# Kernel tuning notes

Measured on AMD Instinct MI355X. Metric: run time of the kernel, lower is better.

## Reference

```python
import jax, jax.numpy as jnp
import numpy as np

EMB = 128  # embsize
WORD = 128  # word_size
ITERS = 2


def _agg(embeds, neibors):
    # embeds: [B, N, D], neibors: [B, N, K] indices into node axis N (per batch)
    # mean-pool gathered neighbor embeddings -> [B, N, D]
    gathered = jax.vmap(lambda e, idx: e[idx])(embeds, neibors)  # [B, N, K, D]
    return gathered.mean(axis=2)


def setup_inputs() -> dict:
    key = jax.random.key(0)
    ks = jax.random.split(key, 9)
    B, N, K = 64, 512, 16
    word_embs = jax.random.normal(ks[0], (B, N, WORD), dtype=jnp.float32)
    lib_embs = jax.random.normal(ks[1], (B, N, WORD), dtype=jnp.float32)
    neibors = jax.random.randint(ks[2], (B, N, K), 0, N)
    neibors_lib = jax.random.randint(ks[3], (B, N, K), 0, N)
    mask = jax.random.uniform(ks[4], (B, N), dtype=jnp.float32)
    # xavier-uniform style params
    def xav(k, shape):
        bound = float(np.sqrt(6.0 / (shape[0] + shape[1])))
        return jax.random.uniform(k, shape, dtype=jnp.float32, minval=-bound, maxval=bound)
    weight = xav(ks[5], (WORD, EMB))
    weight2 = xav(ks[6], (EMB, EMB))
    enc_w1 = xav(ks[7], (WORD, EMB))
    enc_w2 = xav(ks[8], (EMB, EMB))
    return {"word_embs": word_embs, "neibors": neibors, "lib_embs": lib_embs,
            "neibors_lib": neibors_lib, "mask": mask, "weight": weight,
            "weight2": weight2, "enc_w1": enc_w1, "enc_w2": enc_w2}


def reference(word_embs, neibors, lib_embs, neibors_lib, mask, weight, weight2, enc_w1, enc_w2):
    B, N, _ = word_embs.shape
    # lib aggregation is loop-invariant (lib_embs fixed); same math as in-loop recompute
    agg_lib = jnp.einsum('bnw,we->bne', _agg(lib_embs, neibors_lib), weight)  # [B, N, EMB]
    word_proj = jnp.einsum('bnw,we->bne', word_embs, enc_w1)  # loop-invariant
    last_embed = jnp.zeros((B, N, EMB), dtype=jnp.float32)
    for _ in range(ITERS):
        agg_func = _agg(last_embed, neibors)  # [B, N, EMB]
        last_embed = jnp.tanh(word_proj + jnp.einsum('bne,ef->bnf', agg_func, enc_w2) + agg_lib)
    # masked sum over nodes, then final linear
    pooled = (last_embed * mask[:, :, None]).sum(axis=1)  # [B, EMB]
    return pooled @ weight2
```

## Files before the change

kernel.cpp:

```cpp
#include <hip/hip_runtime.h>
#include <hip/hip_bf16.h>

#define B_    64
#define N_    512
#define K_    16
#define D_    128
#define NPBLK 128
#define GG    ((B_*N_)/NPBLK)

typedef float f32x4  __attribute__((ext_vector_type(4)));
typedef short bf16x8 __attribute__((ext_vector_type(8)));

static __device__ __forceinline__ short f2bf(float x) {
    union { float f; unsigned u; } v; v.f = x;
    unsigned r = v.u + 0x7fffu + ((v.u >> 16) & 1u);
    return (short)(r >> 16);
}
static __device__ __forceinline__ float bf2f(short h) {
    return __uint_as_float(((unsigned)(unsigned short)h) << 16);
}
static __device__ __forceinline__ float fast_tanh(float x) {
    float e = __expf(2.f * x);
    return 1.f - 2.f * __builtin_amdgcn_rcpf(e + 1.f);
}

__global__ __launch_bounds__(256) void pack(const float* __restrict__ enc1,
                                            const float* __restrict__ wgt,
                                            const float* __restrict__ enc2,
                                            short* __restrict__ Bp1e,
                                            short* __restrict__ Bpw,
                                            short* __restrict__ Bp2,
                                            float* __restrict__ out) {
    const int blk = blockIdx.x, t = threadIdx.x;
    if (blk >= 24) { out[(blk - 24) * 256 + t] = 0.f; return; }
    const int ptid = blk * 256 + t;
    const int m3 = ptid >> 11;
    const int r = ptid & 2047;
    const int ks = r >> 9, nt = (r >> 6) & 7, l = r & 63;
    const int k0 = ks * 32 + (l >> 4) * 8;
    const int col = nt * 16 + (l & 15);
    const float* src = (m3 == 0) ? enc1 : (m3 == 1) ? wgt : enc2;
    const float scale = (m3 == 0) ? 1.0f : 0.0625f;
    short* dst = (m3 == 0) ? Bp1e : (m3 == 1) ? Bpw : Bp2;
    short o8[8];
#pragma unroll
    for (int j = 0; j < 8; ++j) o8[j] = f2bf(src[(k0 + j) * 128 + col] * scale);
    *(int4*)&dst[(size_t)r * 8] = *(int4*)o8;
}

static __device__ __forceinline__ int swz_blk() {
    const int hw = blockIdx.x;
    return ((hw & 7) << 5) + (hw >> 3);
}

static __device__ __forceinline__ int lds_addr(int row, int colb) {
    return (row * 256 + colb) ^ ((row & 7) << 4);
}

__global__ __launch_bounds__(512, 2) void g1(const float* __restrict__ word,
                                             const int* __restrict__ nbrL,
                                             const float* __restrict__ lib,
                                             const short* __restrict__ Bp1e,
                                             const short* __restrict__ Bpw,
                                             short* __restrict__ baseh,
                                             short* __restrict__ t1g) {
    extern __shared__ char smem[];
    short* sM  = (short*)smem;
    int*  sIdx = (int*)(smem + 131072);
    const int tid = threadIdx.x;
    const int logical = swz_blk();
    const int b = logical >> 2;
    const int node0 = (logical & 3) * NPBLK;
    const int gnode0 = b * N_ + node0;

    const float* libB = lib + (size_t)b * N_ * D_;
#pragma unroll 4
    for (int it = 0; it < 32; ++it) {
        const int i = it * 2048 + tid * 4;
        float4 v = *(const float4*)&libB[i];
        short4 s; s.x = f2bf(v.x); s.y = f2bf(v.y); s.z = f2bf(v.z); s.w = f2bf(v.w);
        *(short4*)(smem + lds_addr(i >> 7, (i & 127) * 2)) = s;
    }
    *(int4*)&sIdx[tid * 4] = *(const int4*)&nbrL[(size_t)gnode0 * 16 + tid * 4];
    __syncthreads();

    const int w = tid >> 6, l = tid & 63;
    const int nrow = w * 16 + (l & 15);
    int nidx[16];
#pragma unroll
    for (int nb = 0; nb < 16; ++nb) nidx[nb] = sIdx[nrow * 16 + nb];

    f32x4 acc[8];
#pragma unroll
    for (int nt = 0; nt < 8; ++nt) acc[nt] = (f32x4)0.f;

    bf16x8 bf[32];
#pragma unroll
    for (int q = 0; q < 32; ++q) bf[q] = *(const bf16x8*)&Bp1e[(size_t)(q * 64 + l) * 8];

    {
        const float* wr = word + (size_t)(gnode0 + nrow) * D_ + (l >> 4) * 8;
#pragma unroll
        for (int ks = 0; ks < 4; ++ks) {
            float4 a0 = *(const float4*)&wr[ks * 32];
            float4 a1 = *(const float4*)&wr[ks * 32 + 4];
            short af[8];
            af[0]=f2bf(a0.x); af[1]=f2bf(a0.y); af[2]=f2bf(a0.z); af[3]=f2bf(a0.w);
            af[4]=f2bf(a1.x); af[5]=f2bf(a1.y); af[6]=f2bf(a1.z); af[7]=f2bf(a1.w);
            bf16x8 av = *(bf16x8*)af;
#pragma unroll
            for (int nt = 0; nt < 8; ++nt)
                acc[nt] = __builtin_amdgcn_mfma_f32_16x16x32_bf16(av, bf[ks * 8 + nt], acc[nt], 0, 0, 0);
        }
    }

#pragma unroll
    for (int q = 0; q < 32; ++q) bf[q] = *(const bf16x8*)&Bpw[(size_t)(q * 64 + l) * 8];

    const int laneoff = (l >> 4) * 16;
#pragma unroll
    for (int nb = 0; nb < 16; ++nb) {
        const int rbase = nidx[nb] * 256 + laneoff;
        const int swz = (nidx[nb] & 7) << 4;
#pragma unroll
        for (int ksq = 0; ksq < 4; ++ksq) {
            bf16x8 av = *(const bf16x8*)(smem + ((rbase + ksq * 64) ^ swz));
#pragma unroll
            for (int nt = 0; nt < 8; ++nt)
                acc[nt] = __builtin_amdgcn_mfma_f32_16x16x32_bf16(av, bf[ksq * 8 + nt], acc[nt], 0, 0, 0);
        }
    }

    const int r0 = w * 16 + (l >> 4) * 4;
    const int cl = l & 15;
#pragma unroll
    for (int nt = 0; nt < 8; ++nt) {
        const int col = nt * 16 + cl;
#pragma unroll
        for (int r = 0; r < 4; ++r) {
            size_t o = (size_t)(gnode0 + r0 + r) * D_ + col;
            float v = acc[nt][r];
            baseh[o] = f2bf(v);
            t1g[o]   = f2bf(fast_tanh(v));
        }
    }
}

__global__ __launch_bounds__(512, 2) void g2(const short* __restrict__ t1g,
                                             const int* __restrict__ nbr,
                                             const short* __restrict__ Bp2,
                                             const short* __restrict__ baseh,
                                             const float* __restrict__ mask,
                                             const float* __restrict__ w2,
                                             float* __restrict__ out) {
    extern __shared__ char smem[];
    short* sM   = (short*)smem;
    int*  sIdx  = (int*)(smem + 131072);
    float* pred = (float*)(smem + 131072 + 8192);
    float* ptot = (float*)(smem + 131072 + 8192 + 4096);
    float* smask= (float*)(smem + 131072 + 8192 + 4096 + 512);
    const int tid = threadIdx.x;
    const int logical = swz_blk();
    const int b = logical >> 2;
    const int node0 = (logical & 3) * NPBLK;
    const int gnode0 = b * N_ + node0;

    const short* tB = t1g + (size_t)b * N_ * D_;
#pragma unroll 4
    for (int it = 0; it < 16; ++it) {
        const int i = it * 4096 + tid * 8;
        int4 v = *(const int4*)&tB[i];
        *(int4*)(smem + lds_addr(i >> 7, (i & 127) * 2)) = v;
    }
    *(int4*)&sIdx[tid * 4] = *(const int4*)&nbr[(size_t)gnode0 * 16 + tid * 4];
    if (tid < 128) smask[tid] = mask[gnode0 + tid];
    __syncthreads();

    const int w = tid >> 6, l = tid & 63;
    const int nrow = w * 16 + (l & 15);
    int nidx[16];
#pragma unroll
    for (int nb = 0; nb < 16; ++nb) nidx[nb] = sIdx[nrow * 16 + nb];

    f32x4 acc[8];
#pragma unroll
    for (int nt = 0; nt < 8; ++nt) acc[nt] = (f32x4)0.f;

    bf16x8 bf[32];
#pragma unroll
    for (int q = 0; q < 32; ++q) bf[q] = *(const bf16x8*)&Bp2[(size_t)(q * 64 + l) * 8];

    const int laneoff = (l >> 4) * 16;
#pragma unroll
    for (int nb = 0; nb < 16; ++nb) {
        const int rbase = nidx[nb] * 256 + laneoff;
        const int swz = (nidx[nb] & 7) << 4;
#pragma unroll
        for (int ksq = 0; ksq < 4; ++ksq) {
            bf16x8 av = *(const bf16x8*)(smem + ((rbase + ksq * 64) ^ swz));
#pragma unroll
            for (int nt = 0; nt < 8; ++nt)
                acc[nt] = __builtin_amdgcn_mfma_f32_16x16x32_bf16(av, bf[ksq * 8 + nt], acc[nt], 0, 0, 0);
        }
    }

    const int r0 = w * 16 + (l >> 4) * 4;
    const int cl = l & 15;
#pragma unroll
    for (int nt = 0; nt < 8; ++nt) {
        const int col = nt * 16 + cl;
        float s = 0.f;
#pragma unroll
        for (int r = 0; r < 4; ++r) {
            size_t o = (size_t)(gnode0 + r0 + r) * D_ + col;
            float v = fast_tanh(bf2f(baseh[o]) + acc[nt][r]);
            s += v * smask[r0 + r];
        }
        s += __shfl_xor(s, 16);
        s += __shfl_xor(s, 32);
        if (l < 16) pred[w * 128 + col] = s;
    }
    __syncthreads();
    if (tid < 128) {
        float tot = 0.f;
#pragma unroll
        for (int i = 0; i < 8; ++i) tot += pred[i * 128 + tid];
        ptot[tid] = tot;
    }
    __syncthreads();
    if (tid < 128) {
        float a2 = 0.f;
#pragma unroll 4
        for (int f = 0; f < 128; ++f) a2 += ptot[f] * w2[f * 128 + tid];
        atomicAdd(&out[b * 128 + tid], a2);
    }
}

extern "C" void kernel_launch(void* const* d_in, const int* in_sizes, int n_in,
                              void* d_out, int out_size, void* d_ws, size_t ws_size,
                              hipStream_t stream) {
    const float* word_embs   = (const float*)d_in[0];
    const int*   neibors     = (const int*)d_in[1];
    const float* lib_embs    = (const float*)d_in[2];
    const int*   neibors_lib = (const int*)d_in[3];
    const float* mask        = (const float*)d_in[4];
    const float* weight      = (const float*)d_in[5];
    const float* weight2     = (const float*)d_in[6];
    const float* enc_w1      = (const float*)d_in[7];
    const float* enc_w2      = (const float*)d_in[8];
    float* out = (float*)d_out;

    char* ws = (char*)d_ws;
    short* baseh = (short*)(ws);
    short* t1g   = (short*)(ws + (1u << 23));
    short* Bp1e  = (short*)(ws + (2u << 23));
    short* Bpw   = (short*)(ws + (2u << 23) + 32768);
    short* Bp2   = (short*)(ws + (2u << 23) + 65536);

    static int attr_done = 0;
    hipFuncSetAttribute((const void*)g1, hipFuncAttributeMaxDynamicSharedMemorySize, 139264);
    hipFuncSetAttribute((const void*)g2, hipFuncAttributeMaxDynamicSharedMemorySize, 144896);
    (void)attr_done;

    pack<<<56, 256, 0, stream>>>(enc_w1, weight, enc_w2, Bp1e, Bpw, Bp2, out);
    g1<<<GG, 512, 139264, stream>>>(word_embs, neibors_lib, lib_embs, Bp1e, Bpw, baseh, t1g);
    g2<<<GG, 512, 144896, stream>>>(t1g, neibors, Bp2, baseh, mask, weight2, out);
}
```

Before: 57.35 us.

## Aggregate neighbors before matmul and premultiply enc_w2 to shrink MFMA work

Uses linearity of the mean to sum gathered neighbor rows with packed fp32 adds first, then multiplies once. Previously every neighbor row was fed through the MFMA. In g1 the word projection and the lib aggregate share one K=256 GEMM. g1 also computes tanh(base)@enc_w2 and stores it, so g2 only gathers, sums, adds base, applies tanh and masks, with no matmul. This cuts MFMA work about 16x, in exchange for scalar gather-add work, an extra bf16 rounding of the intermediate, and B fragments loaded from global inside the loop instead of held in registers.

After: 55.75 us. -2.8%, faster.

```diff
diff --git a/kernel.cpp b/kernel.cpp
--- a/kernel.cpp
+++ b/kernel.cpp
@@ -3,10 +3,7 @@
 
 #define B_    64
 #define N_    512
-#define K_    16
 #define D_    128
-#define NPBLK 128
-#define GG    ((B_*N_)/NPBLK)
 
 typedef float f32x4  __attribute__((ext_vector_type(4)));
 typedef short bf16x8 __attribute__((ext_vector_type(8)));
@@ -16,12 +13,19 @@
     unsigned r = v.u + 0x7fffu + ((v.u >> 16) & 1u);
     return (short)(r >> 16);
 }
+static __device__ __forceinline__ float bfbits2f(unsigned hi_bits) {
+    return __uint_as_float(hi_bits);
+}
 static __device__ __forceinline__ float bf2f(short h) {
     return __uint_as_float(((unsigned)(unsigned short)h) << 16);
 }
 static __device__ __forceinline__ float fast_tanh(float x) {
     float e = __expf(2.f * x);
     return 1.f - 2.f * __builtin_amdgcn_rcpf(e + 1.f);
+}
+static __device__ __forceinline__ void pk_add(float2& acc, float x, float y) {
+    float2 v; v.x = x; v.y = y;
+    asm("v_pk_add_f32 %0, %1, %0" : "+v"(acc) : "v"(v));
 }
 
 __global__ __launch_bounds__(256) void pack(const float* __restrict__ enc1,
@@ -53,84 +57,110 @@
     return ((hw & 7) << 5) + (hw >> 3);
 }
 
-static __device__ __forceinline__ int lds_addr(int row, int colb) {
+static __device__ __forceinline__ int s_addr(int row, int colb) {
     return (row * 256 + colb) ^ ((row & 7) << 4);
 }
+
+#define LDA1 264
+#define LDA2 136
+#define T1OFF 69632
 
 __global__ __launch_bounds__(512, 2) void g1(const float* __restrict__ word,
                                              const int* __restrict__ nbrL,
                                              const float* __restrict__ lib,
                                              const short* __restrict__ Bp1e,
                                              const short* __restrict__ Bpw,
+                                             const short* __restrict__ Bp2,
                                              short* __restrict__ baseh,
-                                             short* __restrict__ t1g) {
+                                             short* __restrict__ u) {
     extern __shared__ char smem[];
-    short* sM  = (short*)smem;
-    int*  sIdx = (int*)(smem + 131072);
     const int tid = threadIdx.x;
     const int logical = swz_blk();
     const int b = logical >> 2;
-    const int node0 = (logical & 3) * NPBLK;
+    const int node0 = (logical & 3) * 128;
     const int gnode0 = b * N_ + node0;
 
     const float* libB = lib + (size_t)b * N_ * D_;
 #pragma unroll 4
-    for (int it = 0; it < 32; ++it) {
-        const int i = it * 2048 + tid * 4;
-        float4 v = *(const float4*)&libB[i];
-        short4 s; s.x = f2bf(v.x); s.y = f2bf(v.y); s.z = f2bf(v.z); s.w = f2bf(v.w);
-        *(short4*)(smem + lds_addr(i >> 7, (i & 127) * 2)) = s;
-    }
-    *(int4*)&sIdx[tid * 4] = *(const int4*)&nbrL[(size_t)gnode0 * 16 + tid * 4];
+    for (int it = 0; it < 16; ++it) {
+        const int i = it * 4096 + tid * 8;
+        float4 v0 = *(const float4*)&libB[i];
+        float4 v1 = *(const float4*)&libB[i + 4];
+        short o8[8];
+        o8[0]=f2bf(v0.x); o8[1]=f2bf(v0.y); o8[2]=f2bf(v0.z); o8[3]=f2bf(v0.w);
+        o8[4]=f2bf(v1.x); o8[5]=f2bf(v1.y); o8[6]=f2bf(v1.z); o8[7]=f2bf(v1.w);
+        *(int4*)(smem + s_addr(i >> 7, (i & 127) * 2)) = *(int4*)o8;
+    }
+    __syncthreads();
+
+    const int row = tid >> 2, cc = tid & 3;
+    int idxv[16];
+#pragma unroll
+    for (int q = 0; q < 4; ++q)
+        *(int4*)&idxv[q * 4] = *(const int4*)&nbrL[(size_t)(gnode0 + row) * 16 + q * 4];
+    float2 ac[16];
+#pragma unroll
+    for (int q = 0; q < 16; ++q) { ac[q].x = 0.f; ac[q].y = 0.f; }
+#pragma unroll
+    for (int nb = 0; nb < 16; ++nb) {
+        const int rr = idxv[nb];
+        const int sbase = rr * 256 + cc * 64;
+        const int sw = (rr & 7) << 4;
+#pragma unroll
+        for (int j = 0; j < 4; ++j) {
+            int4 d = *(const int4*)(smem + ((sbase + j * 16) ^ sw));
+            const unsigned* du = (const unsigned*)&d;
+#pragma unroll
+            for (int q = 0; q < 4; ++q) {
+                pk_add(ac[j * 4 + q], bfbits2f(du[q] << 16), bfbits2f(du[q] & 0xffff0000u));
+            }
+        }
+    }
+    __syncthreads();
+
+    short* sA = (short*)smem;
+    {
+        const float* wr = word + (size_t)(gnode0 + row) * D_ + cc * 32;
+#pragma unroll
+        for (int q = 0; q < 4; ++q) {
+            float4 v0 = *(const float4*)&wr[q * 8];
+            float4 v1 = *(const float4*)&wr[q * 8 + 4];
+            short o8[8];
+            o8[0]=f2bf(v0.x); o8[1]=f2bf(v0.y); o8[2]=f2bf(v0.z); o8[3]=f2bf(v0.w);
+            o8[4]=f2bf(v1.x); o8[5]=f2bf(v1.y); o8[6]=f2bf(v1.z); o8[7]=f2bf(v1.w);
+            *(int4*)&sA[row * LDA1 + cc * 32 + q * 8] = *(int4*)o8;
+        }
+#pragma unroll
+        for (int q = 0; q < 4; ++q) {
+            short o8[8];
+#pragma unroll
+            for (int m = 0; m < 4; ++m) {
+                o8[2*m]   = f2bf(ac[q * 4 + m].x);
+                o8[2*m+1] = f2bf(ac[q * 4 + m].y);
+            }
+            *(int4*)&sA[row * LDA1 + 128 + cc * 32 + q * 8] = *(int4*)o8;
+        }
+    }
     __syncthreads();
 
     const int w = tid >> 6, l = tid & 63;
-    const int nrow = w * 16 + (l & 15);
-    int nidx[16];
-#pragma unroll
-    for (int nb = 0; nb < 16; ++nb) nidx[nb] = sIdx[nrow * 16 + nb];
-
     f32x4 acc[8];
 #pragma unroll
     for (int nt = 0; nt < 8; ++nt) acc[nt] = (f32x4)0.f;
-
-    bf16x8 bf[32];
-#pragma unroll
-    for (int q = 0; q < 32; ++q) bf[q] = *(const bf16x8*)&Bp1e[(size_t)(q * 64 + l) * 8];
-
-    {
-        const float* wr = word + (size_t)(gnode0 + nrow) * D_ + (l >> 4) * 8;
-#pragma unroll
-        for (int ks = 0; ks < 4; ++ks) {
-            float4 a0 = *(const float4*)&wr[ks * 32];
-            float4 a1 = *(const float4*)&wr[ks * 32 + 4];
-            short af[8];
-            af[0]=f2bf(a0.x); af[1]=f2bf(a0.y); af[2]=f2bf(a0.z); af[3]=f2bf(a0.w);
-            af[4]=f2bf(a1.x); af[5]=f2bf(a1.y); af[6]=f2bf(a1.z); af[7]=f2bf(a1.w);
-            bf16x8 av = *(bf16x8*)af;
-#pragma unroll
-            for (int nt = 0; nt < 8; ++nt)
-                acc[nt] = __builtin_amdgcn_mfma_f32_16x16x32_bf16(av, bf[ks * 8 + nt], acc[nt], 0, 0, 0);
-        }
-    }
-
-#pragma unroll
-    for (int q = 0; q < 32; ++q) bf[q] = *(const bf16x8*)&Bpw[(size_t)(q * 64 + l) * 8];
-
-    const int laneoff = (l >> 4) * 16;
-#pragma unroll
-    for (int nb = 0; nb < 16; ++nb) {
-        const int rbase = nidx[nb] * 256 + laneoff;
-        const int swz = (nidx[nb] & 7) << 4;
-#pragma unroll
-        for (int ksq = 0; ksq < 4; ++ksq) {
-            bf16x8 av = *(const bf16x8*)(smem + ((rbase + ksq * 64) ^ swz));
-#pragma unroll
-            for (int nt = 0; nt < 8; ++nt)
-                acc[nt] = __builtin_amdgcn_mfma_f32_16x16x32_bf16(av, bf[ksq * 8 + nt], acc[nt], 0, 0, 0);
-        }
-    }
-
+    const int arow = w * 16 + (l & 15);
+#pragma unroll
+    for (int ks = 0; ks < 8; ++ks) {
+        bf16x8 a = *(const bf16x8*)&sA[arow * LDA1 + ks * 32 + (l >> 4) * 8];
+        const short* bp = (ks < 4) ? &Bp1e[((size_t)(ks * 8) * 64 + l) * 8]
+                                   : &Bpw[((size_t)((ks - 4) * 8) * 64 + l) * 8];
+#pragma unroll
+        for (int nt = 0; nt < 8; ++nt) {
+            bf16x8 bb = *(const bf16x8*)(bp + (size_t)nt * 64 * 8);
+            acc[nt] = __builtin_amdgcn_mfma_f32_16x16x32_bf16(a, bb, acc[nt], 0, 0, 0);
+        }
+    }
+
+    short* t1l = (short*)(smem + T1OFF);
     const int r0 = w * 16 + (l >> 4) * 4;
     const int cl = l & 15;
 #pragma unroll
@@ -138,93 +168,123 @@
         const int col = nt * 16 + cl;
 #pragma unroll
         for (int r = 0; r < 4; ++r) {
-            size_t o = (size_t)(gnode0 + r0 + r) * D_ + col;
+            const int grow = r0 + r;
             float v = acc[nt][r];
-            baseh[o] = f2bf(v);
-            t1g[o]   = f2bf(fast_tanh(v));
-        }
-    }
-}
-
-__global__ __launch_bounds__(512, 2) void g2(const short* __restrict__ t1g,
-                                             const int* __restrict__ nbr,
-                                             const short* __restrict__ Bp2,
+            baseh[(size_t)(gnode0 + grow) * D_ + col] = f2bf(v);
+            t1l[grow * LDA2 + col] = f2bf(fast_tanh(v));
+        }
+    }
+    __syncthreads();
+
+    f32x4 a2[8];
+#pragma unroll
+    for (int nt = 0; nt < 8; ++nt) a2[nt] = (f32x4)0.f;
+#pragma unroll
+    for (int ks = 0; ks < 4; ++ks) {
+        bf16x8 a = *(const bf16x8*)&t1l[arow * LDA2 + ks * 32 + (l >> 4) * 8];
+#pragma unroll
+        for (int nt = 0; nt < 8; ++nt) {
+            bf16x8 bb = *(const bf16x8*)&Bp2[((size_t)(ks * 8 + nt) * 64 + l) * 8];
+            a2[nt] = __builtin_amdgcn_mfma_f32_16x16x32_bf16(a, bb, a2[nt], 0, 0, 0);
+        }
+    }
+#pragma unroll
+    for (int nt = 0; nt < 8; ++nt) {
+        const int col = nt * 16 + cl;
+#pragma unroll
+        for (int r = 0; r < 4; ++r)
+            u[(size_t)(gnode0 + r0 + r) * D_ + col] = f2bf(a2[nt][r]);
+    }
+}
+
+__global__ __launch_bounds__(512, 2) void g2(const int* __restrict__ nbr,
+                                             const short* __restrict__ u,
                                              const short* __restrict__ baseh,
                                              const float* __restrict__ mask,
                                              const float* __restrict__ w2,
                                              float* __restrict__ out) {
     extern __shared__ char smem[];
-    short* sM   = (short*)smem;
-    int*  sIdx  = (int*)(smem + 131072);
-    float* pred = (float*)(smem + 131072 + 8192);
-    float* ptot = (float*)(smem + 131072 + 8192 + 4096);
-    float* smask= (float*)(smem + 131072 + 8192 + 4096 + 512);
     const int tid = threadIdx.x;
     const int logical = swz_blk();
     const int b = logical >> 2;
-    const int node0 = (logical & 3) * NPBLK;
+    const int node0 = (logical & 3) * 128;
     const int gnode0 = b * N_ + node0;
 
-    const short* tB = t1g + (size_t)b * N_ * D_;
+    const short* uB = u + (size_t)b * N_ * D_;
 #pragma unroll 4
     for (int it = 0; it < 16; ++it) {
         const int i = it * 4096 + tid * 8;
-        int4 v = *(const int4*)&tB[i];
-        *(int4*)(smem + lds_addr(i >> 7, (i & 127) * 2)) = v;
-    }
-    *(int4*)&sIdx[tid * 4] = *(const int4*)&nbr[(size_t)gnode0 * 16 + tid * 4];
-    if (tid < 128) smask[tid] = mask[gnode0 + tid];
-    __syncthreads();
-
+        int4 v = *(const int4*)&uB[i];
+        *(int4*)(smem + s_addr(i >> 7, (i & 127) * 2)) = v;
+    }
+    __syncthreads();
+
+    const int row = tid >> 2, cc = tid & 3;
+    int idxv[16];
+#pragma unroll
+    for (int q = 0; q < 4; ++q)
+        *(int4*)&idxv[q * 4] = *(const int4*)&nbr[(size_t)(gnode0 + row) * 16 + q * 4];
+    float2 ac[16];
+#pragma unroll
+    for (int q = 0; q < 16; ++q) { ac[q].x = 0.f; ac[q].y = 0.f; }
+#pragma unroll
+    for (int nb = 0; nb < 16; ++nb) {
+        const int rr = idxv[nb];
+        const int sbase = rr * 256 + cc * 64;
+        const int sw = (rr & 7) << 4;
+#pragma unroll
+        for (int j = 0; j < 4; ++j) {
+            int4 d = *(const int4*)(smem + ((sbase + j * 16) ^ sw));
+            const unsigned* du = (const unsigned*)&d;
+#pragma unroll
+            for (int q = 0; q < 4; ++q) {
+                pk_add(ac[j * 4 + q], bfbits2f(du[q] << 16), bfbits2f(du[q] & 0xffff0000u));
+            }
+        }
+    }
+
+    const float mk = mask[gnode0 + row];
+    {
+        const short* br = &baseh[(size_t)(gnode0 + row) * D_ + cc * 32];
+#pragma unroll
+        for (int q = 0; q < 4; ++q) {
+            int4 bv = *(const int4*)&br[q * 8];
+            const short* bs = (const short*)&bv;
+#pragma unroll
+            for (int m = 0; m < 4; ++m) {
+                ac[q * 4 + m].x = mk * fast_tanh(bf2f(bs[2*m])   + ac[q * 4 + m].x);
+                ac[q * 4 + m].y = mk * fast_tanh(bf2f(bs[2*m+1]) + ac[q * 4 + m].y);
+            }
+        }
+    }
+    __syncthreads();
+
+    float* predp = (float*)smem;
+    float* ptot  = (float*)(smem + 4096);
     const int w = tid >> 6, l = tid & 63;
-    const int nrow = w * 16 + (l & 15);
-    int nidx[16];
-#pragma unroll
-    for (int nb = 0; nb < 16; ++nb) nidx[nb] = sIdx[nrow * 16 + nb];
-
-    f32x4 acc[8];
-#pragma unroll
-    for (int nt = 0; nt < 8; ++nt) acc[nt] = (f32x4)0.f;
-
-    bf16x8 bf[32];
-#pragma unroll
-    for (int q = 0; q < 32; ++q) bf[q] = *(const bf16x8*)&Bp2[(size_t)(q * 64 + l) * 8];
-
-    const int laneoff = (l >> 4) * 16;
-#pragma unroll
-    for (int nb = 0; nb < 16; ++nb) {
-        const int rbase = nidx[nb] * 256 + laneoff;
-        const int swz = (nidx[nb] & 7) << 4;
-#pragma unroll
-        for (int ksq = 0; ksq < 4; ++ksq) {
-            bf16x8 av = *(const bf16x8*)(smem + ((rbase + ksq * 64) ^ swz));
-#pragma unroll
-            for (int nt = 0; nt < 8; ++nt)
-                acc[nt] = __builtin_amdgcn_mfma_f32_16x16x32_bf16(av, bf[ksq * 8 + nt], acc[nt], 0, 0, 0);
-        }
-    }
-
-    const int r0 = w * 16 + (l >> 4) * 4;
-    const int cl = l & 15;
-#pragma unroll
-    for (int nt = 0; nt < 8; ++nt) {
-        const int col = nt * 16 + cl;
-        float s = 0.f;
-#pragma unroll
-        for (int r = 0; r < 4; ++r) {
-            size_t o = (size_t)(gnode0 + r0 + r) * D_ + col;
-            float v = fast_tanh(bf2f(baseh[o]) + acc[nt][r]);
-            s += v * smask[r0 + r];
-        }
-        s += __shfl_xor(s, 16);
-        s += __shfl_xor(s, 32);
-        if (l < 16) pred[w * 128 + col] = s;
+#pragma unroll
+    for (int q = 0; q < 16; ++q) {
+#pragma unroll
+        for (int st = 4; st <= 32; st <<= 1) {
+            ac[q].x += __shfl_xor(ac[q].x, st);
+            ac[q].y += __shfl_xor(ac[q].y, st);
+        }
+    }
+    if (l < 4) {
+#pragma unroll
+        for (int q = 0; q < 4; ++q) {
+#pragma unroll
+            for (int m = 0; m < 4; ++m) {
+                predp[w * 128 + l * 32 + q * 8 + m * 2]     = ac[q * 4 + m].x;
+                predp[w * 128 + l * 32 + q * 8 + m * 2 + 1] = ac[q * 4 + m].y;
+            }
+        }
     }
     __syncthreads();
     if (tid < 128) {
         float tot = 0.f;
 #pragma unroll
-        for (int i = 0; i < 8; ++i) tot += pred[i * 128 + tid];
+        for (int i = 0; i < 8; ++i) tot += predp[i * 128 + tid];
         ptot[tid] = tot;
     }
     __syncthreads();
@@ -252,17 +312,15 @@
 
     char* ws = (char*)d_ws;
     short* baseh = (short*)(ws);
-    short* t1g   = (short*)(ws + (1u << 23));
+    short* ubuf  = (short*)(ws + (1u << 23));
     short* Bp1e  = (short*)(ws + (2u << 23));
     short* Bpw   = (short*)(ws + (2u << 23) + 32768);
     short* Bp2   = (short*)(ws + (2u << 23) + 65536);
 
-    static int attr_done = 0;
-    hipFuncSetAttribute((const void*)g1, hipFuncAttributeMaxDynamicSharedMemorySize, 139264);
-    hipFuncSetAttribute((const void*)g2, hipFuncAttributeMaxDynamicSharedMemorySize, 144896);
-    (void)attr_done;
+    hipFuncSetAttribute((const void*)g1, hipFuncAttributeMaxDynamicSharedMemorySize, 131072);
+    hipFuncSetAttribute((const void*)g2, hipFuncAttributeMaxDynamicSharedMemorySize, 131072);
 
     pack<<<56, 256, 0, stream>>>(enc_w1, weight, enc_w2, Bp1e, Bpw, Bp2, out);
-    g1<<<GG, 512, 139264, stream>>>(word_embs, neibors_lib, lib_embs, Bp1e, Bpw, baseh, t1g);
-    g2<<<GG, 512, 144896, stream>>>(t1g, neibors, Bp2, baseh, mask, weight2, out);
-}
+    g1<<<256, 512, 131072, stream>>>(word_embs, neibors_lib, lib_embs, Bp1e, Bpw, Bp2, baseh, ubuf);
+    g2<<<256, 512, 131072, stream>>>(neibors, ubuf, baseh, mask, weight2, out);
+}
```
